# Performance work log

Measured on AMD Instinct MI355X. Metric: run time of the kernel, lower is better.

## Reference

```python
import jax, jax.numpy as jnp
import numpy as np

C = 2048
EPS = 1e-12


def conv1x1(x, w, b):
    # x: [B,C_in,H,W], w: [C_out,C_in], b: [C_out]
    return jnp.einsum('oc,bchw->bohw', w, x) + b[None, :, None, None]


def unfold3x3(x):
    # torch F.unfold(kernel=3, padding=1): output [B, C*9, H*W],
    # feature order (c, ki, kj) with c slowest.
    B, Cc, H, W = x.shape
    xp = jnp.pad(x, ((0, 0), (0, 0), (1, 1), (1, 1)))
    patches = jnp.stack([xp[:, :, ki:ki + H, kj:kj + W]
                         for ki in range(3) for kj in range(3)], axis=2)  # [B,C,9,H,W]
    return patches.reshape(B, Cc * 9, H * W)


def fold3x3(u, H, W):
    # torch F.fold(kernel=3, padding=1): overlap-add. u: [B, C*9, H*W]
    B = u.shape[0]
    Cc = u.shape[1] // 9
    t = u.reshape(B, Cc, 3, 3, H, W)
    out = jnp.zeros((B, Cc, H + 2, W + 2), dtype=u.dtype)
    for ki in range(3):
        for kj in range(3):
            out = out.at[:, :, ki:ki + H, kj:kj + W].add(t[:, :, ki, kj])
    return out[:, :, 1:1 + H, 1:1 + W]


def l2norm(x, axis):
    n = jnp.sqrt(jnp.sum(x * x, axis=axis, keepdims=True))
    return x / jnp.maximum(n, EPS)


def setup_inputs() -> dict:
    key = jax.random.key(0)
    ks = jax.random.split(key, 8)
    B, H, W = 4, 24, 24
    s = 0.02
    return {
        'part_ref': jax.random.normal(ks[0], (B, C, H, W), jnp.float32),
        'part_target': jax.random.normal(ks[1], (B, C, H, W), jnp.float32),
        'wq': jax.random.normal(ks[2], (C, C), jnp.float32) * s,
        'bq': jnp.zeros((C,), jnp.float32),
        'wk': jax.random.normal(ks[3], (C, C), jnp.float32) * s,
        'bk': jnp.zeros((C,), jnp.float32),
        'wt': jax.random.normal(ks[4], (C, 2 * C), jnp.float32) * s,
        'bt': jnp.zeros((C,), jnp.float32),
    }


def reference(part_ref, part_target, wq, bq, wk, bk, wt, bt):
    B, _, H, W = part_ref.shape
    part_target_o = part_target
    k = conv1x1(part_ref, wk, bk)
    q = conv1x1(part_target, wq, bq)

    tgt_unf = unfold3x3(q)        # [B, C*9, L]
    ref_unf1 = unfold3x3(k)       # [B, C*9, L]

    ref_n = l2norm(jnp.transpose(ref_unf1, (0, 2, 1)), axis=2)  # [B, L, C*9]
    tgt_n = l2norm(tgt_unf, axis=1)                              # [B, C*9, L]

    R = jnp.einsum('blc,bcm->blm', ref_n, tgt_n)  # [B, L_ref, L_tgt]
    R_star = jnp.max(R, axis=1)                   # [B, L]
    R_arg = jnp.argmax(R, axis=1)                 # [B, L]

    # gather best ref patch per target location along dim 2
    T_unf = jnp.take_along_axis(ref_unf1, R_arg[:, None, :], axis=2)  # [B, C*9, L]
    T_part = fold3x3(T_unf, H, W) / 9.0

    S = R_star.reshape(B, 1, H, W)
    x_res = jnp.concatenate((q, T_part), axis=1)  # [B, 2C, H, W]
    res = conv1x1(x_res, wt, bt) * S + part_target_o
    return res
```

## Files before the change

### kernel.cpp

```cpp
#include <hip/hip_runtime.h>
#include <cstddef>
#include <cstdint>

#define LPIX 576
#define CCH  2048
#define NB   4

typedef __attribute__((ext_vector_type(8))) short short8;
typedef __attribute__((ext_vector_type(4))) float f32x4;
typedef __attribute__((ext_vector_type(4))) unsigned short u16x4;

__device__ __forceinline__ unsigned short f2bf(float f) {
    uint32_t u = __builtin_bit_cast(uint32_t, f);
    u += 0x7fff + ((u >> 16) & 1);
    return (unsigned short)(u >> 16);
}
__device__ __forceinline__ float bf2f(unsigned short s) {
    return __builtin_bit_cast(float, (uint32_t)s << 16);
}

__device__ __forceinline__ void gload_lds16(const void* g, void* l) {
    __builtin_amdgcn_global_load_lds((const __attribute__((address_space(1))) void*)g,
                                     (__attribute__((address_space(3))) void*)l, 16, 0, 0);
}

template<int BM, int BN>
__device__ __forceinline__ void mm_core64(
    const short* __restrict__ Ab, int lda,
    const short* __restrict__ Bb, int ldb,
    int k0, int kend, short* As, short* Bs,
    int m0, int n0, f32x4 (&acc)[BM/32][BN/32])
{
    const int tid  = threadIdx.x;
    const int lane = tid & 63;
    const int w    = tid >> 6;
    const int wm = (w & 1) * (BM / 2);
    const int wn = (w >> 1) * (BN / 2);
    const int l15 = lane & 15;
    const int k8  = (lane >> 4) * 8;
    const int r   = tid >> 2;
    const int kk  = (tid & 3) * 8;

    const short* Aptr[BM / 32]; short* Alds[BM / 32];
    #pragma unroll
    for (int u = 0; u < BM / 32; ++u) {
        const int p = u & 1, g = u >> 1;
        Aptr[u] = Ab + (size_t)(m0 + g * 64 + r) * lda + p * 32 + kk;
        Alds[u] = As + p * BM * 32 + g * 2048 + tid * 8;
    }
    const short* Bptr[BN / 32]; short* Blds[BN / 32];
    #pragma unroll
    for (int u = 0; u < BN / 32; ++u) {
        const int p = u & 1, g = u >> 1;
        Bptr[u] = Bb + (size_t)(n0 + g * 64 + r) * ldb + p * 32 + kk;
        Blds[u] = Bs + p * BN * 32 + g * 2048 + tid * 8;
    }

    for (int c0 = k0; c0 < kend; c0 += 64) {
        #pragma unroll
        for (int u = 0; u < BM / 32; ++u) gload_lds16(Aptr[u] + c0, Alds[u]);
        #pragma unroll
        for (int u = 0; u < BN / 32; ++u) gload_lds16(Bptr[u] + c0, Blds[u]);
        __syncthreads();
        #pragma unroll
        for (int s = 0; s < 2; ++s) {
            short8 fa[BM / 32], fb[BN / 32];
            #pragma unroll
            for (int i = 0; i < BM / 32; ++i)
                fa[i] = *(const short8*)(As + s * BM * 32 + (wm + i * 16 + l15) * 32 + k8);
            #pragma unroll
            for (int j = 0; j < BN / 32; ++j)
                fb[j] = *(const short8*)(Bs + s * BN * 32 + (wn + j * 16 + l15) * 32 + k8);
            #pragma unroll
            for (int i = 0; i < BM / 32; ++i)
                #pragma unroll
                for (int j = 0; j < BN / 32; ++j)
                    acc[i][j] = __builtin_amdgcn_mfma_f32_16x16x32_bf16(fa[i], fb[j], acc[i][j], 0, 0, 0);
        }
        __syncthreads();
    }
}

__global__ __launch_bounds__(256) void wcast2_k(const float* __restrict__ wq,
                                                const float* __restrict__ wk,
                                                short* __restrict__ Wb) {
    const float* W = blockIdx.y ? wk : wq;
    short* D = Wb + (size_t)blockIdx.y * CCH * CCH;
    int i = (blockIdx.x * 256 + threadIdx.x) * 4;
    float4 v = *(const float4*)(W + i);
    u16x4 u;
    u.x = f2bf(v.x); u.y = f2bf(v.y); u.z = f2bf(v.z); u.w = f2bf(v.w);
    *(u16x4*)(D + i) = u;
}

__global__ __launch_bounds__(256) void wcast_k(const float* __restrict__ W,
                                               short* __restrict__ Wb) {
    int i = (blockIdx.x * 256 + threadIdx.x) * 4;
    float4 v = *(const float4*)(W + i);
    u16x4 u;
    u.x = f2bf(v.x); u.y = f2bf(v.y); u.z = f2bf(v.z); u.w = f2bf(v.w);
    *(u16x4*)(Wb + i) = u;
}

__global__ __launch_bounds__(256) void tcast_k(const float* __restrict__ tgt,
                                               const float* __restrict__ ref,
                                               short* __restrict__ T1) {
    __shared__ float tile[32][33];
    const int z = blockIdx.z;
    const int b = z & 3, which = z >> 2;
    const float* X = (which ? ref : tgt) + (size_t)b * CCH * LPIX;
    const int c0 = blockIdx.y * 32;
    const int l0 = blockIdx.x * 32;
    const int tx = threadIdx.x, ty = threadIdx.y;
    #pragma unroll
    for (int j = 0; j < 4; ++j)
        tile[ty + j * 8][tx] = X[(size_t)(c0 + ty + j * 8) * LPIX + l0 + tx];
    __syncthreads();
    short* D = T1 + ((size_t)(which * NB + b) * LPIX) * CCH;
    #pragma unroll
    for (int j = 0; j < 4; ++j)
        D[(size_t)(l0 + ty + j * 8) * CCH + c0 + tx] = (short)f2bf(tile[tx][ty + j * 8]);
}

__global__ __launch_bounds__(256) void conv_k(
    const short* __restrict__ T1, const short* __restrict__ Wb,
    const float* __restrict__ bq, const float* __restrict__ bk,
    short* __restrict__ x2t, short* __restrict__ kt)
{
    __shared__ short As[64 * 64];
    __shared__ short Bs[128 * 64];
    const int z = blockIdx.z;
    const int b = z >> 1, which = z & 1;
    const short* Ab = T1 + (size_t)(which * NB + b) * LPIX * CCH;
    const short* Bb = Wb + (size_t)which * CCH * CCH;
    const float* bias = which ? bk : bq;
    short* Yb = which ? (kt + (size_t)b * LPIX * CCH) : (x2t + (size_t)b * LPIX * 4096);
    const int ldy = which ? CCH : 4096;
    const int m0 = blockIdx.y * 64;
    const int n0 = blockIdx.x * 128;
    f32x4 acc[2][4] = {};
    mm_core64<64, 128>(Ab, CCH, Bb, CCH, 0, CCH, As, Bs, m0, n0, acc);
    const int lane = threadIdx.x & 63, w = threadIdx.x >> 6;
    const int wm = (w & 1) * 32, wn = (w >> 1) * 64;
    const int l15 = lane & 15, quad = lane >> 4;
    #pragma unroll
    for (int i = 0; i < 2; ++i)
        #pragma unroll
        for (int j = 0; j < 4; ++j) {
            const int gn = n0 + wn + j * 16 + l15;
            const float bi = bias[gn];
            #pragma unroll
            for (int r = 0; r < 4; ++r) {
                const int gm = m0 + wm + i * 16 + quad * 4 + r;
                Yb[(size_t)gm * ldy + gn] = (short)f2bf(acc[i][j][r] + bi);
            }
        }
}

__global__ __launch_bounds__(256) void gram_k(
    const short* __restrict__ kt, const short* __restrict__ x2t,
    float* __restrict__ Mpart)
{
    __shared__ short As[64 * 64];
    __shared__ short Bs[64 * 64];
    const int z = blockIdx.z;
    const int b = z >> 1, kc = z & 1;
    const short* Ab = kt + (size_t)b * LPIX * CCH;
    const short* Bb = x2t + (size_t)b * LPIX * 4096;
    const int m0 = blockIdx.y * 64;
    const int n0 = blockIdx.x * 64;
    f32x4 acc[2][2] = {};
    mm_core64<64, 64>(Ab, CCH, Bb, 4096, kc * 1024, kc * 1024 + 1024, As, Bs, m0, n0, acc);
    float* Mb = Mpart + (size_t)(kc * NB + b) * LPIX * LPIX;
    const int lane = threadIdx.x & 63, w = threadIdx.x >> 6;
    const int wm = (w & 1) * 32, wn = (w >> 1) * 32;
    const int l15 = lane & 15, quad = lane >> 4;
    #pragma unroll
    for (int i = 0; i < 2; ++i)
        #pragma unroll
        for (int j = 0; j < 2; ++j) {
            const int gn = n0 + wn + j * 16 + l15;
            #pragma unroll
            for (int r = 0; r < 4; ++r) {
                const int gm = m0 + wm + i * 16 + quad * 4 + r;
                Mb[(size_t)gm * LPIX + gn] = acc[i][j][r];
            }
        }
}

__global__ __launch_bounds__(256) void fin_k(
    const short* __restrict__ wtb, const short* __restrict__ x2t,
    const float* __restrict__ bt, const float* __restrict__ S,
    const float* __restrict__ PT, float* __restrict__ out)
{
    __shared__ short As[128 * 64];
    __shared__ short Bs[64 * 64];
    const int b = blockIdx.z;
    const short* Bb = x2t + (size_t)b * LPIX * 4096;
    const int m0 = blockIdx.y * 128;
    const int n0 = blockIdx.x * 64;
    f32x4 acc[4][2] = {};
    mm_core64<128, 64>(wtb, 4096, Bb, 4096, 0, 4096, As, Bs, m0, n0, acc);
    const int lane = threadIdx.x & 63, w = threadIdx.x >> 6;
    const int wm = (w & 1) * 64, wn = (w >> 1) * 32;
    const int l15 = lane & 15, quad = lane >> 4;
    #pragma unroll
    for (int i = 0; i < 4; ++i)
        #pragma unroll
        for (int j = 0; j < 2; ++j) {
            const int gn = n0 + wn + j * 16 + l15;
            const float sv = S[b * LPIX + gn];
            #pragma unroll
            for (int r = 0; r < 4; ++r) {
                const int gm = m0 + wm + i * 16 + quad * 4 + r;
                float v = (acc[i][j][r] + bt[gm]) * sv
                        + PT[((size_t)b * CCH + gm) * LPIX + gn];
                out[((size_t)b * CCH + gm) * LPIX + gn] = v;
            }
        }
}

__global__ __launch_bounds__(256) void sqnorm_k(
    const short* __restrict__ qt, const short* __restrict__ kt,
    float* __restrict__ nq, float* __restrict__ nk)
{
    const int b = blockIdx.y;
    const int l = blockIdx.x * 4 + threadIdx.y;
    const int lane = threadIdx.x;
    const int z = blockIdx.z;
    const short* src = z ? (kt + ((size_t)b * LPIX + l) * CCH)
                         : (qt + ((size_t)b * LPIX + l) * 4096);
    float s = 0.f;
    #pragma unroll
    for (int j = 0; j < 8; ++j) {
        u16x4 u = *(const u16x4*)(src + (lane + j * 64) * 4);
        float a = bf2f(u.x), c = bf2f(u.y), d = bf2f(u.z), e = bf2f(u.w);
        s += a * a + c * c + d * d + e * e;
    }
    #pragma unroll
    for (int off = 32; off > 0; off >>= 1)
        s += __shfl_down(s, off);
    if (lane == 0) (z ? nk : nq)[b * LPIX + l] = s;
}

__global__ void boxinv_k(const float* __restrict__ nk, const float* __restrict__ nq,
                         float* __restrict__ invNk, float* __restrict__ invNq)
{
    int idx = blockIdx.x * 256 + threadIdx.x;
    if (idx >= 2 * NB * LPIX) return;
    int map = idx / (NB * LPIX);
    int rem = idx % (NB * LPIX);
    int b = rem / LPIX, l = rem % LPIX;
    int i = l / 24, j = l % 24;
    const float* src = map ? nq : nk;
    float s = 0.f;
    for (int di = -1; di <= 1; ++di)
        for (int dj = -1; dj <= 1; ++dj) {
            int ii = i + di, jj = j + dj;
            if (ii >= 0 && ii < 24 && jj >= 0 && jj < 24)
                s += src[b * LPIX + ii * 24 + jj];
        }
    float n = fmaxf(sqrtf(s), 1e-12f);
    (map ? invNq : invNk)[b * LPIX + l] = 1.0f / n;
}

__global__ __launch_bounds__(256) void argmax1_k(
    const float* __restrict__ Mpart, const float* __restrict__ invNk,
    float* __restrict__ Pv, int* __restrict__ Pi)
{
    const int b   = blockIdx.z;
    const int lrb = blockIdx.y;
    const int tx = threadIdx.x, ty = threadIdx.y;
    const int lt = blockIdx.x * 64 + tx;
    const int it = lt / 24, jt = lt % 24;
    const float* Mb0 = Mpart + (size_t)b * LPIX * LPIX;
    const float* Mb1 = Mpart + (size_t)(NB + b) * LPIX * LPIX;
    float best = -1e30f; int bidx = 0;
    #pragma unroll
    for (int i = 0; i < 6; ++i) {
        const int lr = lrb * 24 + ty + i * 4;
        const int ir = lr / 24, jr = lr % 24;
        const int base = lr * LPIX + lt;
        float g = 0.f;
        #pragma unroll
        for (int di = -1; di <= 1; ++di) {
            if ((unsigned)(ir + di) > 23u || (unsigned)(it + di) > 23u) continue;
            #pragma unroll
            for (int dj = -1; dj <= 1; ++dj) {
                if ((unsigned)(jr + dj) > 23u || (unsigned)(jt + dj) > 23u) continue;
                const int o = base + (di * 24 + dj) * (LPIX + 1);
                g += Mb0[o] + Mb1[o];
            }
        }
        float v = g * invNk[b * LPIX + lr];
        if (v > best) { best = v; bidx = lr; }
    }
    __shared__ float rv[4][64];
    __shared__ int   ri[4][64];
    rv[ty][tx] = best; ri[ty][tx] = bidx;
    __syncthreads();
    if (ty == 0) {
        #pragma unroll
        for (int y = 1; y < 4; ++y) {
            float v = rv[y][tx]; int id = ri[y][tx];
            if (v > best || (v == best && id < bidx)) { best = v; bidx = id; }
        }
        Pv[((size_t)b * 24 + lrb) * LPIX + lt] = best;
        Pi[((size_t)b * 24 + lrb) * LPIX + lt] = bidx;
    }
}

__global__ __launch_bounds__(256) void argmax2_k(
    const float* __restrict__ Pv, const int* __restrict__ Pi,
    const float* __restrict__ invNq,
    float* __restrict__ S, int* __restrict__ Arg)
{
    int idx = blockIdx.x * 256 + threadIdx.x;
    if (idx >= NB * LPIX) return;
    int b = idx / LPIX, lt = idx % LPIX;
    float best = -1e30f; int bidx = 0;
    #pragma unroll
    for (int c = 0; c < 24; ++c) {
        float v = Pv[((size_t)b * 24 + c) * LPIX + lt];
        int  id = Pi[((size_t)b * 24 + c) * LPIX + lt];
        if (v > best || (v == best && id < bidx)) { best = v; bidx = id; }
    }
    S[idx]   = best * invNq[idx];
    Arg[idx] = bidx;
}

__global__ __launch_bounds__(256) void gather_k(
    const short* __restrict__ kt, const int* __restrict__ Arg,
    short* __restrict__ x2t)
{
    const int b = blockIdx.y;
    const int l0 = blockIdx.x * 4;
    const int lane = threadIdx.x, ty = threadIdx.y;
    const int tid = ty * 64 + lane;
    __shared__ int tap[4][9];
    if (tid < 36) {
        int px = tid / 9, t9 = tid % 9;
        int l = l0 + px;
        int i = l / 24, j = l % 24;
        int ki = t9 / 3, kj = t9 % 3;
        int ip = i + 1 - ki, jp = j + 1 - kj;
        int off = -1;
        if (ip >= 0 && ip < 24 && jp >= 0 && jp < 24) {
            int a = Arg[b * LPIX + ip * 24 + jp];
            int rr = a / 24 + ki - 1;
            int cc = a % 24 + kj - 1;
            if (rr >= 0 && rr < 24 && cc >= 0 && cc < 24) off = rr * 24 + cc;
        }
        tap[px][t9] = off;
    }
    __syncthreads();
    const int l = l0 + ty;
    const short* Kb = kt + (size_t)b * LPIX * CCH;
    short* dst = x2t + ((size_t)b * LPIX + l) * 4096 + CCH;
    int t[9];
    #pragma unroll
    for (int i = 0; i < 9; ++i) t[i] = tap[ty][i];
    const float inv9 = 1.0f / 9.0f;
    #pragma unroll
    for (int j = 0; j < 8; ++j) {
        int c = (lane + j * 64) * 4;
        float s0 = 0.f, s1 = 0.f, s2 = 0.f, s3 = 0.f;
        #pragma unroll
        for (int t9 = 0; t9 < 9; ++t9) {
            int off = t[t9];
            if (off < 0) continue;
            u16x4 u = *(const u16x4*)(Kb + (size_t)off * CCH + c);
            s0 += bf2f(u.x); s1 += bf2f(u.y); s2 += bf2f(u.z); s3 += bf2f(u.w);
        }
        u16x4 o;
        o.x = f2bf(s0 * inv9); o.y = f2bf(s1 * inv9);
        o.z = f2bf(s2 * inv9); o.w = f2bf(s3 * inv9);
        *(u16x4*)(dst + c) = o;
    }
}

extern "C" void kernel_launch(void* const* d_in, const int* in_sizes, int n_in,
                              void* d_out, int out_size, void* d_ws, size_t ws_size,
                              hipStream_t stream) {
    const float* part_ref = (const float*)d_in[0];
    const float* part_tgt = (const float*)d_in[1];
    const float* wq = (const float*)d_in[2];
    const float* bq = (const float*)d_in[3];
    const float* wk = (const float*)d_in[4];
    const float* bk = (const float*)d_in[5];
    const float* wt = (const float*)d_in[6];
    const float* bt = (const float*)d_in[7];
    float* out = (float*)d_out;

    short* wqb2 = (short*)d_ws;
    short* wtb  = wqb2;
    short* T1   = wqb2 + (size_t)2 * CCH * CCH;
    short* kt   = T1 + (size_t)2 * NB * LPIX * CCH;
    short* x2t  = kt + (size_t)NB * LPIX * CCH;
    float* Mpart = (float*)T1;
    float* nk    = (float*)(x2t + (size_t)NB * LPIX * 4096);
    float* nq    = nk + NB * LPIX;
    float* invNk = nq + NB * LPIX;
    float* invNq = invNk + NB * LPIX;
    float* Sbuf  = invNq + NB * LPIX;
    int*   Arg   = (int*)(Sbuf + NB * LPIX);
    float* Pv    = (float*)(Arg + NB * LPIX);
    int*   Pi    = (int*)(Pv + (size_t)24 * NB * LPIX);

    wcast2_k<<<dim3(4096, 2), 256, 0, stream>>>(wq, wk, wqb2);
    tcast_k<<<dim3(18, 64, 8), dim3(32, 8), 0, stream>>>(part_tgt, part_ref, T1);

    conv_k<<<dim3(16, 9, 8), 256, 0, stream>>>(T1, wqb2, bq, bk, x2t, kt);

    sqnorm_k<<<dim3(144, NB, 2), dim3(64, 4), 0, stream>>>(x2t, kt, nq, nk);
    boxinv_k<<<18, 256, 0, stream>>>(nk, nq, invNk, invNq);

    gram_k<<<dim3(9, 9, 8), 256, 0, stream>>>(kt, x2t, Mpart);

    argmax1_k<<<dim3(9, 24, NB), dim3(64, 4), 0, stream>>>(Mpart, invNk, Pv, Pi);
    argmax2_k<<<9, 256, 0, stream>>>(Pv, Pi, invNq, Sbuf, Arg);

    gather_k<<<dim3(144, NB), dim3(64, 4), 0, stream>>>(kt, Arg, x2t);

    wcast_k<<<8192, 256, 0, stream>>>(wt, wtb);
    fin_k<<<dim3(9, 16, 4), 256, 0, stream>>>(wtb, x2t, bt, Sbuf, part_tgt, out);
}
```

Baseline: 365.4 us.

## Fuse squared norms into conv epilogue and remap blocks for XCD locality

Computes per-pixel squared norms inside the conv epilogue with shuffle reductions and atomics, removing the separate sqnorm and box-inverse kernels. The 3x3 box-sum of norms is moved into argmax1 and argmax2. conv, gather and fin now use a flattened grid whose block IDs are remapped so that blocks sharing weights or batch data land on the same XCD, aiming for better L2 reuse. This adds a memset, atomics (summation order is no longer deterministic) and the squared norms are now taken from fp32 values rather than bf16-rounded ones.

```diff
diff --git a/kernel.cpp b/kernel.cpp
--- a/kernel.cpp
+++ b/kernel.cpp
@@ -125,24 +125,31 @@
 __global__ __launch_bounds__(256) void conv_k(
     const short* __restrict__ T1, const short* __restrict__ Wb,
     const float* __restrict__ bq, const float* __restrict__ bk,
-    short* __restrict__ x2t, short* __restrict__ kt)
+    short* __restrict__ x2t, short* __restrict__ kt,
+    float* __restrict__ nq, float* __restrict__ nk)
 {
     __shared__ short As[64 * 64];
     __shared__ short Bs[128 * 64];
-    const int z = blockIdx.z;
-    const int b = z >> 1, which = z & 1;
+    const int id = blockIdx.x;
+    const int xcd = id & 7, slot = id >> 3;
+    const int sid = xcd * 4 + slot / 36;
+    const int r36 = slot % 36;
+    const int which = sid >> 4;
+    const int m0 = (r36 % 9) * 64;
+    const int n0 = (sid & 15) * 128;
+    const int b  = r36 / 9;
     const short* Ab = T1 + (size_t)(which * NB + b) * LPIX * CCH;
     const short* Bb = Wb + (size_t)which * CCH * CCH;
     const float* bias = which ? bk : bq;
     short* Yb = which ? (kt + (size_t)b * LPIX * CCH) : (x2t + (size_t)b * LPIX * 4096);
+    float* Nb = (which ? nk : nq) + b * LPIX;
     const int ldy = which ? CCH : 4096;
-    const int m0 = blockIdx.y * 64;
-    const int n0 = blockIdx.x * 128;
     f32x4 acc[2][4] = {};
     mm_core64<64, 128>(Ab, CCH, Bb, CCH, 0, CCH, As, Bs, m0, n0, acc);
     const int lane = threadIdx.x & 63, w = threadIdx.x >> 6;
     const int wm = (w & 1) * 32, wn = (w >> 1) * 64;
     const int l15 = lane & 15, quad = lane >> 4;
+    float pv[2][4] = {};
     #pragma unroll
     for (int i = 0; i < 2; ++i)
         #pragma unroll
@@ -152,7 +159,21 @@
             #pragma unroll
             for (int r = 0; r < 4; ++r) {
                 const int gm = m0 + wm + i * 16 + quad * 4 + r;
-                Yb[(size_t)gm * ldy + gn] = (short)f2bf(acc[i][j][r] + bi);
+                float v = acc[i][j][r] + bi;
+                pv[i][r] += v * v;
+                Yb[(size_t)gm * ldy + gn] = (short)f2bf(v);
+            }
+        }
+    #pragma unroll
+    for (int i = 0; i < 2; ++i)
+        #pragma unroll
+        for (int r = 0; r < 4; ++r) {
+            float s = pv[i][r];
+            #pragma unroll
+            for (int m = 1; m < 16; m <<= 1) s += __shfl_xor(s, m);
+            if (l15 == 0) {
+                const int gm = m0 + wm + i * 16 + quad * 4 + r;
+                atomicAdd(&Nb[gm], s);
             }
         }
 }
@@ -195,10 +216,14 @@
 {
     __shared__ short As[128 * 64];
     __shared__ short Bs[64 * 64];
-    const int b = blockIdx.z;
+    const int id = blockIdx.x;
+    const int xcd = id & 7, slot = id >> 3;
+    const int hi = slot >= 36;
+    const int r36 = slot - hi * 36;
+    const int m0 = (xcd * 2 + hi) * 128;
+    const int n0 = (r36 % 9) * 64;
+    const int b  = r36 / 9;
     const short* Bb = x2t + (size_t)b * LPIX * 4096;
-    const int m0 = blockIdx.y * 128;
-    const int n0 = blockIdx.x * 64;
     f32x4 acc[4][2] = {};
     mm_core64<128, 64>(wtb, 4096, Bb, 4096, 0, 4096, As, Bs, m0, n0, acc);
     const int lane = threadIdx.x & 63, w = threadIdx.x >> 6;
@@ -220,57 +245,32 @@
         }
 }
 
-__global__ __launch_bounds__(256) void sqnorm_k(
-    const short* __restrict__ qt, const short* __restrict__ kt,
-    float* __restrict__ nq, float* __restrict__ nk)
-{
-    const int b = blockIdx.y;
-    const int l = blockIdx.x * 4 + threadIdx.y;
-    const int lane = threadIdx.x;
-    const int z = blockIdx.z;
-    const short* src = z ? (kt + ((size_t)b * LPIX + l) * CCH)
-                         : (qt + ((size_t)b * LPIX + l) * 4096);
-    float s = 0.f;
-    #pragma unroll
-    for (int j = 0; j < 8; ++j) {
-        u16x4 u = *(const u16x4*)(src + (lane + j * 64) * 4);
-        float a = bf2f(u.x), c = bf2f(u.y), d = bf2f(u.z), e = bf2f(u.w);
-        s += a * a + c * c + d * d + e * e;
-    }
-    #pragma unroll
-    for (int off = 32; off > 0; off >>= 1)
-        s += __shfl_down(s, off);
-    if (lane == 0) (z ? nk : nq)[b * LPIX + l] = s;
-}
-
-__global__ void boxinv_k(const float* __restrict__ nk, const float* __restrict__ nq,
-                         float* __restrict__ invNk, float* __restrict__ invNq)
-{
-    int idx = blockIdx.x * 256 + threadIdx.x;
-    if (idx >= 2 * NB * LPIX) return;
-    int map = idx / (NB * LPIX);
-    int rem = idx % (NB * LPIX);
-    int b = rem / LPIX, l = rem % LPIX;
-    int i = l / 24, j = l % 24;
-    const float* src = map ? nq : nk;
-    float s = 0.f;
-    for (int di = -1; di <= 1; ++di)
-        for (int dj = -1; dj <= 1; ++dj) {
-            int ii = i + di, jj = j + dj;
-            if (ii >= 0 && ii < 24 && jj >= 0 && jj < 24)
-                s += src[b * LPIX + ii * 24 + jj];
-        }
-    float n = fmaxf(sqrtf(s), 1e-12f);
-    (map ? invNq : invNk)[b * LPIX + l] = 1.0f / n;
-}
-
 __global__ __launch_bounds__(256) void argmax1_k(
-    const float* __restrict__ Mpart, const float* __restrict__ invNk,
+    const float* __restrict__ Mpart, const float* __restrict__ nk,
     float* __restrict__ Pv, int* __restrict__ Pi)
 {
     const int b   = blockIdx.z;
     const int lrb = blockIdx.y;
     const int tx = threadIdx.x, ty = threadIdx.y;
+    const int tid = ty * 64 + tx;
+    __shared__ float invNkS[24];
+    if (tid < 24) {
+        const int jr = tid;
+        float s = 0.f;
+        #pragma unroll
+        for (int di = -1; di <= 1; ++di) {
+            const int ii = lrb + di;
+            if ((unsigned)ii > 23u) continue;
+            #pragma unroll
+            for (int dj = -1; dj <= 1; ++dj) {
+                const int jj = jr + dj;
+                if ((unsigned)jj > 23u) continue;
+                s += nk[b * LPIX + ii * 24 + jj];
+            }
+        }
+        invNkS[jr] = 1.0f / fmaxf(sqrtf(s), 1e-12f);
+    }
+    __syncthreads();
     const int lt = blockIdx.x * 64 + tx;
     const int it = lt / 24, jt = lt % 24;
     const float* Mb0 = Mpart + (size_t)b * LPIX * LPIX;
@@ -278,13 +278,13 @@
     float best = -1e30f; int bidx = 0;
     #pragma unroll
     for (int i = 0; i < 6; ++i) {
-        const int lr = lrb * 24 + ty + i * 4;
-        const int ir = lr / 24, jr = lr % 24;
+        const int jr = ty + i * 4;
+        const int lr = lrb * 24 + jr;
         const int base = lr * LPIX + lt;
         float g = 0.f;
         #pragma unroll
         for (int di = -1; di <= 1; ++di) {
-            if ((unsigned)(ir + di) > 23u || (unsigned)(it + di) > 23u) continue;
+            if ((unsigned)(lrb + di) > 23u || (unsigned)(it + di) > 23u) continue;
             #pragma unroll
             for (int dj = -1; dj <= 1; ++dj) {
                 if ((unsigned)(jr + dj) > 23u || (unsigned)(jt + dj) > 23u) continue;
@@ -292,7 +292,7 @@
                 g += Mb0[o] + Mb1[o];
             }
         }
-        float v = g * invNk[b * LPIX + lr];
+        float v = g * invNkS[jr];
         if (v > best) { best = v; bidx = lr; }
     }
     __shared__ float rv[4][64];
@@ -312,12 +312,26 @@
 
 __global__ __launch_bounds__(256) void argmax2_k(
     const float* __restrict__ Pv, const int* __restrict__ Pi,
-    const float* __restrict__ invNq,
+    const float* __restrict__ nq,
     float* __restrict__ S, int* __restrict__ Arg)
 {
     int idx = blockIdx.x * 256 + threadIdx.x;
     if (idx >= NB * LPIX) return;
     int b = idx / LPIX, lt = idx % LPIX;
+    int it = lt / 24, jt = lt % 24;
+    float s = 0.f;
+    #pragma unroll
+    for (int di = -1; di <= 1; ++di) {
+        const int ii = it + di;
+        if ((unsigned)ii > 23u) continue;
+        #pragma unroll
+        for (int dj = -1; dj <= 1; ++dj) {
+            const int jj = jt + dj;
+            if ((unsigned)jj > 23u) continue;
+            s += nq[b * LPIX + ii * 24 + jj];
+        }
+    }
+    const float invNq = 1.0f / fmaxf(sqrtf(s), 1e-12f);
     float best = -1e30f; int bidx = 0;
     #pragma unroll
     for (int c = 0; c < 24; ++c) {
@@ -325,7 +339,7 @@
         int  id = Pi[((size_t)b * 24 + c) * LPIX + lt];
         if (v > best || (v == best && id < bidx)) { best = v; bidx = id; }
     }
-    S[idx]   = best * invNq[idx];
+    S[idx]   = best * invNq;
     Arg[idx] = bidx;
 }
 
@@ -333,8 +347,10 @@
     const short* __restrict__ kt, const int* __restrict__ Arg,
     short* __restrict__ x2t)
 {
-    const int b = blockIdx.y;
-    const int l0 = blockIdx.x * 4;
+    const int id = blockIdx.x;
+    const int xcd = id & 7, slot = id >> 3;
+    const int b  = xcd >> 1;
+    const int l0 = ((xcd & 1) * 72 + slot) * 4;
     const int lane = threadIdx.x, ty = threadIdx.y;
     const int tid = ty * 64 + lane;
     __shared__ int tap[4][9];
@@ -400,28 +416,25 @@
     float* Mpart = (float*)T1;
     float* nk    = (float*)(x2t + (size_t)NB * LPIX * 4096);
     float* nq    = nk + NB * LPIX;
-    float* invNk = nq + NB * LPIX;
-    float* invNq = invNk + NB * LPIX;
-    float* Sbuf  = invNq + NB * LPIX;
+    float* Sbuf  = nq + NB * LPIX;
     int*   Arg   = (int*)(Sbuf + NB * LPIX);
     float* Pv    = (float*)(Arg + NB * LPIX);
     int*   Pi    = (int*)(Pv + (size_t)24 * NB * LPIX);
 
+    hipMemsetAsync(nk, 0, 2 * NB * LPIX * sizeof(float), stream);
+
     wcast2_k<<<dim3(4096, 2), 256, 0, stream>>>(wq, wk, wqb2);
     tcast_k<<<dim3(18, 64, 8), dim3(32, 8), 0, stream>>>(part_tgt, part_ref, T1);
 
-    conv_k<<<dim3(16, 9, 8), 256, 0, stream>>>(T1, wqb2, bq, bk, x2t, kt);
-
-    sqnorm_k<<<dim3(144, NB, 2), dim3(64, 4), 0, stream>>>(x2t, kt, nq, nk);
-    boxinv_k<<<18, 256, 0, stream>>>(nk, nq, invNk, invNq);
+    conv_k<<<1152, 256, 0, stream>>>(T1, wqb2, bq, bk, x2t, kt, nq, nk);
 
     gram_k<<<dim3(9, 9, 8), 256, 0, stream>>>(kt, x2t, Mpart);
 
-    argmax1_k<<<dim3(9, 24, NB), dim3(64, 4), 0, stream>>>(Mpart, invNk, Pv, Pi);
-    argmax2_k<<<9, 256, 0, stream>>>(Pv, Pi, invNq, Sbuf, Arg);
-
-    gather_k<<<dim3(144, NB), dim3(64, 4), 0, stream>>>(kt, Arg, x2t);
+    argmax1_k<<<dim3(9, 24, NB), dim3(64, 4), 0, stream>>>(Mpart, nk, Pv, Pi);
+    argmax2_k<<<9, 256, 0, stream>>>(Pv, Pi, nq, Sbuf, Arg);
+
+    gather_k<<<576, dim3(64, 4), 0, stream>>>(kt, Arg, x2t);
 
     wcast_k<<<8192, 256, 0, stream>>>(wt, wtb);
-    fin_k<<<dim3(9, 16, 4), 256, 0, stream>>>(wtb, x2t, bt, Sbuf, part_tgt, out);
-}
+    fin_k<<<576, 256, 0, stream>>>(wtb, x2t, bt, Sbuf, part_tgt, out);
+}
```

Measured after the change: 351.6 us. 3.8% less time.
